# Optimization experiments

Hardware: AMD Instinct MI355X
Metric: run time of the kernel (lower is better)

The kernel has to match this reference:

```python
import jax, jax.numpy as jnp
import numpy as np

N = 50000          # num nodes
E = 1_000_000      # num edges
H = 64             # hidden_dim
IMG, TWT, NUMP, CAT = 512, 768, 16, 8
NCLS, NET = 2, 3   # num_classes, num_edge_types


def setup_inputs() -> dict:
    key = jax.random.key(0)
    ks = jax.random.split(key, 40)
    f32 = jnp.float32
    w = lambda k, s: (jax.random.normal(k, s, f32) * 0.02)
    inp = {
        # forward args
        "image": jax.random.normal(ks[0], (N, IMG), f32),
        "tweets": jax.random.normal(ks[1], (N, TWT), f32),
        "num_prop": jax.random.normal(ks[2], (N, NUMP), f32),
        "category": jax.random.normal(ks[3], (N, CAT), f32),
        "edge_index": jax.random.randint(ks[4], (2, E), 0, N, jnp.int32),
        "edge_type": jax.random.randint(ks[5], (E,), 0, NET, jnp.int32),
        # explicit randomness (replaces randn_like / Bernoulli.sample)
        "eps": jax.random.normal(ks[6], (E, H), f32),
        "u": jax.random.uniform(ks[7], (E,), f32),
        # parameters (stored [in, out]; y = x @ W + b)
        "Wi": w(ks[8], (IMG, H)), "bi": jnp.zeros((H,), f32),
        "Wt": w(ks[9], (TWT, H)), "bt": jnp.zeros((H,), f32),
        "Wn": w(ks[10], (NUMP, H)), "bn": jnp.zeros((H,), f32),
        "Wc": w(ks[11], (CAT, H)), "bc": jnp.zeros((H,), f32),
        "Wf": w(ks[12], (4 * H, H)), "bf": jnp.zeros((H,), f32),
        "Eet": w(ks[13], (NET, 2 * H)),              # edge_type_embed
        "Wmu": w(ks[14], (2 * H, H)), "bmu": jnp.zeros((H,), f32),
        "Wlv": w(ks[15], (2 * H, H)), "blv": jnp.zeros((H,), f32),
        "Wm1": w(ks[16], (2 * H, 64)), "bm1": jnp.zeros((64,), f32),
        "Wm2": w(ks[17], (64, 1)), "bm2": jnp.zeros((1,), f32),
        "Wcls": w(ks[18], (H, NCLS)), "bcls": jnp.zeros((NCLS,), f32),
    }
    return inp


def reference(image, tweets, num_prop, category, edge_index, edge_type, eps, u,
              Wi, bi, Wt, bt, Wn, bn, Wc, bc, Wf, bf, Eet,
              Wmu, bmu, Wlv, blv, Wm1, bm1, Wm2, bm2, Wcls, bcls):
    relu = jax.nn.relu
    # encode_user
    img_f = relu(image @ Wi + bi)
    twt_f = relu(tweets @ Wt + bt)
    num_f = relu(num_prop @ Wn + bn)
    cat_f = relu(category @ Wc + bc)
    node_features = relu(jnp.concatenate([img_f, twt_f, num_f, cat_f], -1) @ Wf + bf)  # [N, H]

    src, dst = edge_index[0], edge_index[1]
    u_i, u_j = node_features[src], node_features[dst]          # [E, H] each
    edge_emb = relu(jnp.concatenate([u_i, u_j], -1) + Eet[edge_type])  # [E, 2H]

    # parameterized_gaussian (z unused downstream, kept for fidelity)
    mu = edge_emb @ Wmu + bmu
    log_var = edge_emb @ Wlv + blv
    z = mu + eps * jnp.exp(0.5 * log_var)

    # edge confidence + Bernoulli sample via inverse-CDF with provided uniforms
    logits_e = (relu(edge_emb @ Wm1 + bm1) @ Wm2 + bm2)[:, 0]  # [E]
    p_ij = jax.nn.sigmoid(logits_e)
    s = (u < p_ij).astype(node_features.dtype)                 # trusted-edge indicator, [E]

    # segment-mean of dst features over trusted edges, grouped by src
    sums = jax.ops.segment_sum(u_j * s[:, None], src, num_segments=N)  # [N, H]
    cnt = jax.ops.segment_sum(s, src, num_segments=N)                  # [N]
    agg = jnp.where(cnt[:, None] > 0, sums / jnp.maximum(cnt, 1.0)[:, None], node_features)

    return agg @ Wcls + bcls  # [N, num_classes]
```

## Files before the change

kernel.cpp:

```cpp
#include <hip/hip_runtime.h>
#include <cstdint>

typedef short short8 __attribute__((ext_vector_type(8)));
typedef float f32x4  __attribute__((ext_vector_type(4)));

__device__ __forceinline__ void split2(float x, short& h, short& l) {
  unsigned u  = __float_as_uint(x);
  unsigned rh = u + 0x7FFFu + ((u >> 16) & 1u);
  h = (short)(rh >> 16);
  float hf = __uint_as_float((rh >> 16) << 16);
  float lf = x - hf;
  unsigned ul = __float_as_uint(lf);
  unsigned rl = ul + 0x7FFFu + ((ul >> 16) & 1u);
  l = (short)(rl >> 16);
}

__device__ __forceinline__ void split4(float4 a, uint2& hp, uint2& lp) {
  unsigned hp0, hp1, lp0, lp1;
  asm("v_cvt_pk_bf16_f32 %0, %1, %2" : "=v"(hp0) : "v"(a.x), "v"(a.y));
  asm("v_cvt_pk_bf16_f32 %0, %1, %2" : "=v"(hp1) : "v"(a.z), "v"(a.w));
  float h0 = __uint_as_float(hp0 << 16);
  float h1 = __uint_as_float(hp0 & 0xFFFF0000u);
  float h2 = __uint_as_float(hp1 << 16);
  float h3 = __uint_as_float(hp1 & 0xFFFF0000u);
  float l0 = a.x - h0, l1 = a.y - h1, l2 = a.z - h2, l3 = a.w - h3;
  asm("v_cvt_pk_bf16_f32 %0, %1, %2" : "=v"(lp0) : "v"(l0), "v"(l1));
  asm("v_cvt_pk_bf16_f32 %0, %1, %2" : "=v"(lp1) : "v"(l2), "v"(l3));
  hp = make_uint2(hp0, hp1);
  lp = make_uint2(lp0, lp1);
}

__global__ __launch_bounds__(256) void init_head(int* __restrict__ head, int N)
{
  const int i = blockIdx.x * 256 + threadIdx.x;
  if (i < N) head[i] = -1;
}

__global__ __launch_bounds__(256) void prep_w(
    const float* __restrict__ Wi, const float* __restrict__ Wt,
    const float* __restrict__ Wn, const float* __restrict__ Wc,
    const float* __restrict__ Wf, const float* __restrict__ Wm1,
    short* __restrict__ hi, short* __restrict__ lo)
{
  int idx = blockIdx.x * 256 + threadIdx.x;
  if (idx >= 1728 * 64) return;
  int kp = idx >> 6, col = idx & 63;
  const float* W; int K, kloc, base;
  if (kp < 512)       { W = Wi;            K = 512; kloc = kp;        base = 0;    }
  else if (kp < 1280) { W = Wt;            K = 768; kloc = kp - 512;  base = 512;  }
  else if (kp < 1312) { W = Wn;            K = 16;  kloc = kp - 1280; base = 1280; }
  else if (kp < 1344) { W = Wc;            K = 8;   kloc = kp - 1312; base = 1312; }
  else if (kp < 1600) { W = Wf;            K = 256; kloc = kp - 1344; base = 1344; }
  else if (kp < 1664) { W = Wm1;           K = 64;  kloc = kp - 1600; base = 1600; }
  else                { W = Wm1 + 64 * 64; K = 64;  kloc = kp - 1664; base = 1664; }
  float x = (kloc < K) ? W[(size_t)kloc * 64 + col] : 0.f;
  short h, l; split2(x, h, l);
  int s = kloc >> 5;
  int addr = ((s * 4 + (col >> 4)) * 64 + ((col & 15) | (((kloc >> 3) & 3) << 4))) * 8 + (kloc & 7);
  size_t o = (size_t)base * 64 + addr;
  hi[o] = h; lo[o] = l;
}

__global__ __launch_bounds__(256) void encoder(
    const float* __restrict__ image, const float* __restrict__ tweets,
    const float* __restrict__ nump, const float* __restrict__ catg,
    const short* __restrict__ Whi, const short* __restrict__ Wlo,
    const float* __restrict__ bi, const float* __restrict__ bt,
    const float* __restrict__ bn, const float* __restrict__ bc,
    const float* __restrict__ bf, float* __restrict__ nf, int M)
{
  __shared__ short Ahi[2][2048];
  __shared__ short Alo[2][2048];
  __shared__ float htile[64 * 68];
  const int tid  = threadIdx.x;
  const int m0   = blockIdx.x * 64;
  const int w    = tid >> 6, l = tid & 63;
  const int srow = tid >> 3;
  const int k0   = (tid & 7) * 4;
  const int i0   = k0 & 7;
  const int kg   = k0 >> 3;

  f32x4 acc2[4];
#pragma unroll
  for (int n = 0; n < 4; n++) acc2[n] = (f32x4){0.f, 0.f, 0.f, 0.f};

  auto stage = [&](const float* A, int lda, int K, int s, int buf) {
#pragma unroll
    for (int r2 = 0; r2 < 2; r2++) {
      const int row  = srow + r2 * 32;
      const int grow = m0 + row;
      const int k    = s * 32 + k0;
      float4 a = make_float4(0.f, 0.f, 0.f, 0.f);
      if (grow < M && k < K) {
        if (k + 3 < K) {
          a = *reinterpret_cast<const float4*>(A + (size_t)grow * lda + k);
        } else {
          a.x = A[(size_t)grow * lda + k];
        }
      }
      uint2 hp, lp; split4(a, hp, lp);
      const int addr = (row >> 4) * 512 + (((row & 15) | (kg << 4)) * 8 + i0);
      *reinterpret_cast<uint2*>(&Ahi[buf][addr]) = hp;
      *reinterpret_cast<uint2*>(&Alo[buf][addr]) = lp;
    }
  };

  auto do_segment = [&](const float* A, int lda, int K, int ksteps,
                        int wstep0, const float* bias, int seg) {
    f32x4 acc[4];
#pragma unroll
    for (int n = 0; n < 4; n++) acc[n] = (f32x4){0.f, 0.f, 0.f, 0.f};

    stage(A, lda, K, 0, 0);
    for (int s = 0; s < ksteps; s++) {
      __syncthreads();
      if (s + 1 < ksteps) stage(A, lda, K, s + 1, (s + 1) & 1);
      const int buf = s & 1;
      short8 ahi = *reinterpret_cast<const short8*>(&Ahi[buf][w * 512 + l * 8]);
      short8 alo = *reinterpret_cast<const short8*>(&Alo[buf][w * 512 + l * 8]);
#pragma unroll
      for (int n = 0; n < 4; n++) {
        short8 whi = *reinterpret_cast<const short8*>(&Whi[((size_t)(wstep0 + s) * 4 + n) * 512 + l * 8]);
        short8 wlo = *reinterpret_cast<const short8*>(&Wlo[((size_t)(wstep0 + s) * 4 + n) * 512 + l * 8]);
        acc[n] = __builtin_amdgcn_mfma_f32_16x16x32_bf16(ahi, whi, acc[n], 0, 0, 0);
        acc[n] = __builtin_amdgcn_mfma_f32_16x16x32_bf16(alo, whi, acc[n], 0, 0, 0);
        acc[n] = __builtin_amdgcn_mfma_f32_16x16x32_bf16(ahi, wlo, acc[n], 0, 0, 0);
      }
    }
    __syncthreads();

#pragma unroll
    for (int n = 0; n < 4; n++) {
      const int c  = n * 16 + (l & 15);
      const float bb = bias[c];
#pragma unroll
      for (int j = 0; j < 4; j++) {
        const int row = w * 16 + (l >> 4) * 4 + j;
        htile[row * 68 + c] = fmaxf(acc[n][j] + bb, 0.f);
      }
    }
    __syncthreads();

#pragma unroll
    for (int ks2 = 0; ks2 < 2; ks2++) {
#pragma unroll
      for (int r2 = 0; r2 < 2; r2++) {
        const int row = srow + r2 * 32;
        float4 a = *reinterpret_cast<const float4*>(&htile[row * 68 + ks2 * 32 + k0]);
        uint2 hp, lp; split4(a, hp, lp);
        const int addr = (row >> 4) * 512 + (((row & 15) | (kg << 4)) * 8 + i0);
        *reinterpret_cast<uint2*>(&Ahi[ks2][addr]) = hp;
        *reinterpret_cast<uint2*>(&Alo[ks2][addr]) = lp;
      }
    }
    __syncthreads();

#pragma unroll
    for (int ks2 = 0; ks2 < 2; ks2++) {
      short8 ahi = *reinterpret_cast<const short8*>(&Ahi[ks2][w * 512 + l * 8]);
      short8 alo = *reinterpret_cast<const short8*>(&Alo[ks2][w * 512 + l * 8]);
      const int st = 42 + seg * 2 + ks2;
#pragma unroll
      for (int n = 0; n < 4; n++) {
        short8 whi = *reinterpret_cast<const short8*>(&Whi[((size_t)st * 4 + n) * 512 + l * 8]);
        short8 wlo = *reinterpret_cast<const short8*>(&Wlo[((size_t)st * 4 + n) * 512 + l * 8]);
        acc2[n] = __builtin_amdgcn_mfma_f32_16x16x32_bf16(ahi, whi, acc2[n], 0, 0, 0);
        acc2[n] = __builtin_amdgcn_mfma_f32_16x16x32_bf16(alo, whi, acc2[n], 0, 0, 0);
        acc2[n] = __builtin_amdgcn_mfma_f32_16x16x32_bf16(ahi, wlo, acc2[n], 0, 0, 0);
      }
    }
    __syncthreads();
  };

  do_segment(image,  512, 512, 16, 0,  bi, 0);
  do_segment(tweets, 768, 768, 24, 16, bt, 1);
  do_segment(nump,   16,  16,  1,  40, bn, 2);
  do_segment(catg,   8,   8,   1,  41, bc, 3);

  const int rb  = m0 + w * 16 + (l >> 4) * 4;
  const int c15 = l & 15;
#pragma unroll
  for (int n = 0; n < 4; n++) {
    const int c = n * 16 + c15;
    const float bb = bf[c];
#pragma unroll
    for (int j = 0; j < 4; j++) {
      const int r = rb + j;
      if (r < M) nf[(size_t)r * 64 + c] = fmaxf(acc2[n][j] + bb, 0.f);
    }
  }
}

__global__ __launch_bounds__(256) void table_kernel(
    const float* __restrict__ nf, const float* __restrict__ Eet,
    const short* __restrict__ Whi, const short* __restrict__ Wlo,
    const float* __restrict__ bm1,
    float* __restrict__ Atab, float* __restrict__ Btab, int N3, int gT)
{
  const bool isB    = (int)blockIdx.x >= gT;
  const int  m0     = (isB ? (int)blockIdx.x - gT : (int)blockIdx.x) * 64;
  const int  eoff   = isB ? 64 : 0;
  const int  wstep0 = isB ? 52 : 50;
  float*     Tab    = isB ? Btab : Atab;

  __shared__ short Ahi[2][2048];
  __shared__ short Alo[2][2048];
  const int tid  = threadIdx.x;
  const int w    = tid >> 6, l = tid & 63;
  const int srow = tid >> 3;
  const int k0   = (tid & 7) * 4;
  const int i0   = k0 & 7;
  const int kg   = k0 >> 3;

#pragma unroll
  for (int ks2 = 0; ks2 < 2; ks2++) {
#pragma unroll
    for (int r2 = 0; r2 < 2; r2++) {
      const int row = srow + r2 * 32;
      const int rg  = m0 + row;
      float4 v = make_float4(0.f, 0.f, 0.f, 0.f);
      if (rg < N3) {
        const int n = rg / 3;
        const int t = rg - n * 3;
        const int k = ks2 * 32 + k0;
        float4 x = *reinterpret_cast<const float4*>(&nf[(size_t)n * 64 + k]);
        float4 e = *reinterpret_cast<const float4*>(&Eet[(size_t)t * 128 + eoff + k]);
        v.x = fmaxf(x.x + e.x, 0.f); v.y = fmaxf(x.y + e.y, 0.f);
        v.z = fmaxf(x.z + e.z, 0.f); v.w = fmaxf(x.w + e.w, 0.f);
      }
      uint2 hp, lp; split4(v, hp, lp);
      const int addr = (row >> 4) * 512 + (((row & 15) | (kg << 4)) * 8 + i0);
      *reinterpret_cast<uint2*>(&Ahi[ks2][addr]) = hp;
      *reinterpret_cast<uint2*>(&Alo[ks2][addr]) = lp;
    }
  }
  __syncthreads();

  f32x4 acc[4];
#pragma unroll
  for (int n = 0; n < 4; n++) acc[n] = (f32x4){0.f, 0.f, 0.f, 0.f};

#pragma unroll
  for (int ks2 = 0; ks2 < 2; ks2++) {
    short8 ahi = *reinterpret_cast<const short8*>(&Ahi[ks2][w * 512 + l * 8]);
    short8 alo = *reinterpret_cast<const short8*>(&Alo[ks2][w * 512 + l * 8]);
#pragma unroll
    for (int n = 0; n < 4; n++) {
      short8 whi = *reinterpret_cast<const short8*>(&Whi[((size_t)(wstep0 + ks2) * 4 + n) * 512 + l * 8]);
      short8 wlo = *reinterpret_cast<const short8*>(&Wlo[((size_t)(wstep0 + ks2) * 4 + n) * 512 + l * 8]);
      acc[n] = __builtin_amdgcn_mfma_f32_16x16x32_bf16(ahi, whi, acc[n], 0, 0, 0);
      acc[n] = __builtin_amdgcn_mfma_f32_16x16x32_bf16(alo, whi, acc[n], 0, 0, 0);
      acc[n] = __builtin_amdgcn_mfma_f32_16x16x32_bf16(ahi, wlo, acc[n], 0, 0, 0);
    }
  }

  const int rb  = m0 + w * 16 + (l >> 4) * 4;
  const int c15 = l & 15;
#pragma unroll
  for (int n = 0; n < 4; n++) {
    const int c = n * 16 + c15;
    const float bb = isB ? 0.f : bm1[c];
#pragma unroll
    for (int j = 0; j < 4; j++) {
      const int r = rb + j;
      if (r < N3) Tab[(size_t)r * 64 + c] = acc[n][j] + bb;
    }
  }
}

__global__ __launch_bounds__(256) void edge_kernel(
    const int* __restrict__ ei, const int* __restrict__ et,
    const float* __restrict__ u,
    const float* __restrict__ Atab, const float* __restrict__ Btab,
    const float* __restrict__ Wm2, const float* __restrict__ bm2,
    int* __restrict__ head, int* __restrict__ nxt, int E)
{
  const int tid = threadIdx.x;
  const int e   = blockIdx.x * 16 + (tid >> 4);
  const int sub = tid & 15;
  if (e >= E) return;

  const int sn = ei[e];
  const int dn = ei[E + e];
  const int t  = et[e];

  float4 a  = *reinterpret_cast<const float4*>(Atab + ((size_t)sn * 3 + t) * 64 + sub * 4);
  float4 b  = *reinterpret_cast<const float4*>(Btab + ((size_t)dn * 3 + t) * 64 + sub * 4);
  float4 wv = *reinterpret_cast<const float4*>(Wm2 + sub * 4);

  float v = fmaxf(a.x + b.x, 0.f) * wv.x;
  v = fmaf(fmaxf(a.y + b.y, 0.f), wv.y, v);
  v = fmaf(fmaxf(a.z + b.z, 0.f), wv.z, v);
  v = fmaf(fmaxf(a.w + b.w, 0.f), wv.w, v);
  v += __shfl_xor(v, 1);
  v += __shfl_xor(v, 2);
  v += __shfl_xor(v, 4);
  v += __shfl_xor(v, 8);

  if (sub == 0) {
    const float p = 1.f / (1.f + expf(-(v + bm2[0])));
    if (u[e] < p) {
      nxt[e] = atomicExch(&head[sn], e);
    }
  }
}

__global__ __launch_bounds__(256) void node_kernel(
    const int* __restrict__ head, const int* __restrict__ nxt,
    const int* __restrict__ ei,
    const float* __restrict__ nf,
    const float* __restrict__ Wcls, const float* __restrict__ bcls,
    float* __restrict__ out, int N, int E)
{
  const int n    = (int)((blockIdx.x * (unsigned)blockDim.x + threadIdx.x) >> 6);
  const int lane = threadIdx.x & 63;
  if (n >= N) return;

  double acc = 0.0;
  int    c   = 0;
  int    e   = head[n];
  while (e >= 0) {
    const int dn = ei[E + e];
    acc += (double)nf[(size_t)dn * 64 + lane];
    c++;
    e = nxt[e];
  }

  const float agg = (c > 0) ? (float)(acc / (double)c) : nf[(size_t)n * 64 + lane];
  float r0 = agg * Wcls[lane * 2 + 0];
  float r1 = agg * Wcls[lane * 2 + 1];
#pragma unroll
  for (int off = 32; off; off >>= 1) {
    r0 += __shfl_xor(r0, off, 64);
    r1 += __shfl_xor(r1, off, 64);
  }
  if (lane == 0) {
    out[(size_t)n * 2 + 0] = r0 + bcls[0];
    out[(size_t)n * 2 + 1] = r1 + bcls[1];
  }
}

extern "C" void kernel_launch(void* const* d_in, const int* in_sizes, int n_in,
                              void* d_out, int out_size, void* d_ws, size_t ws_size,
                              hipStream_t stream)
{
  const float* image    = (const float*)d_in[0];
  const float* tweets   = (const float*)d_in[1];
  const float* num_prop = (const float*)d_in[2];
  const float* category = (const float*)d_in[3];
  const int*   ei       = (const int*)  d_in[4];
  const int*   et       = (const int*)  d_in[5];
  const float* u        = (const float*)d_in[7];
  const float* Wi  = (const float*)d_in[8],  *bi  = (const float*)d_in[9];
  const float* Wt  = (const float*)d_in[10], *bt  = (const float*)d_in[11];
  const float* Wn  = (const float*)d_in[12], *bn  = (const float*)d_in[13];
  const float* Wc  = (const float*)d_in[14], *bc  = (const float*)d_in[15];
  const float* Wf  = (const float*)d_in[16], *bf  = (const float*)d_in[17];
  const float* Eet = (const float*)d_in[18];
  const float* Wm1 = (const float*)d_in[23], *bm1 = (const float*)d_in[24];
  const float* Wm2 = (const float*)d_in[25], *bm2 = (const float*)d_in[26];
  const float* Wcls= (const float*)d_in[27], *bcls= (const float*)d_in[28];
  float* out = (float*)d_out;

  const int N = in_sizes[0] / 512;
  const int E = in_sizes[5];

  float* ws = (float*)d_ws;
  size_t off = 0;
  float* nf     = ws + off;  off += (size_t)N * 64;
  float* Atab   = ws + off;  off += (size_t)N * 3 * 64;
  float* Btab   = ws + off;  off += (size_t)N * 3 * 64;
  int*   head   = (int*)(ws + off);  off += (size_t)N;
  int*   nxt    = (int*)(ws + off);  off += (size_t)E;
  short* Wfhi   = (short*)(ws + off);  off += (1728 * 64) / 2;
  short* Wflo   = (short*)(ws + off);  off += (1728 * 64) / 2;

  init_head<<<(N + 255) / 256, 256, 0, stream>>>(head, N);

  prep_w<<<(1728 * 64 + 255) / 256, 256, 0, stream>>>(Wi, Wt, Wn, Wc, Wf, Wm1,
                                                      Wfhi, Wflo);

  const int gN = (N + 63) / 64;
  encoder<<<gN, 256, 0, stream>>>(image, tweets, num_prop, category,
                                  Wfhi, Wflo, bi, bt, bn, bc, bf, nf, N);

  const int N3 = N * 3;
  const int gT = (N3 + 63) / 64;
  table_kernel<<<2 * gT, 256, 0, stream>>>(nf, Eet, Wfhi, Wflo, bm1,
                                           Atab, Btab, N3, gT);

  edge_kernel<<<(E + 15) / 16, 256, 0, stream>>>(ei, et, u, Atab, Btab,
                                                 Wm2, bm2, head, nxt, E);

  node_kernel<<<(N + 3) / 4, 256, 0, stream>>>(head, nxt, ei, nf, Wcls, bcls,
                                               out, N, E);
}
```

Measured before the change: 328.8 us.

## Pipeline encoder loads via async global-to-LDS copies with four-stage ring buffer

Restructures the encoder GEMM so the raw fp32 input tiles and the pre-split bf16 weight tiles are copied straight into LDS with global_load_lds, using a four-slot ring buffer kept two steps ahead and explicit vmcnt waits. The four input segments are merged into a single 42-step loop. The fp32-to-bf16 hi/lo split now happens after the LDS read instead of before the LDS write, and the rows are XOR-swizzled to avoid bank conflicts. The aim is to hide global memory latency and remove register staging and extra barriers. In exchange it uses 80KB of LDS, which limits occupancy, and it relies on hand-tuned waitcnt counts.

```diff
diff --git a/kernel.cpp b/kernel.cpp
--- a/kernel.cpp
+++ b/kernel.cpp
@@ -28,6 +28,12 @@
   asm("v_cvt_pk_bf16_f32 %0, %1, %2" : "=v"(lp1) : "v"(l2), "v"(l3));
   hp = make_uint2(hp0, hp1);
   lp = make_uint2(lp0, lp1);
+}
+
+__device__ __forceinline__ void gl_lds16(const void* g, void* l) {
+  __builtin_amdgcn_global_load_lds(
+      (const __attribute__((address_space(1))) unsigned int*)g,
+      (__attribute__((address_space(3))) unsigned int*)l, 16, 0, 0);
 }
 
 __global__ __launch_bounds__(256) void init_head(int* __restrict__ head, int N)
@@ -61,6 +67,12 @@
   hi[o] = h; lo[o] = l;
 }
 
+#define ENC_STEPS 42
+#define A_OFF   0
+#define W_OFF   32768
+#define HHI_OFF 65536
+#define HLO_OFF 73728
+
 __global__ __launch_bounds__(256) void encoder(
     const float* __restrict__ image, const float* __restrict__ tweets,
     const float* __restrict__ nump, const float* __restrict__ catg,
@@ -69,96 +81,66 @@
     const float* __restrict__ bn, const float* __restrict__ bc,
     const float* __restrict__ bf, float* __restrict__ nf, int M)
 {
-  __shared__ short Ahi[2][2048];
-  __shared__ short Alo[2][2048];
-  __shared__ float htile[64 * 68];
+  __shared__ uint4 smem4[81920 / 16];
+  char* lds = (char*)smem4;
+
   const int tid  = threadIdx.x;
   const int m0   = blockIdx.x * 64;
   const int w    = tid >> 6, l = tid & 63;
-  const int srow = tid >> 3;
-  const int k0   = (tid & 7) * 4;
-  const int i0   = k0 & 7;
-  const int kg   = k0 >> 3;
-
-  f32x4 acc2[4];
-#pragma unroll
-  for (int n = 0; n < 4; n++) acc2[n] = (f32x4){0.f, 0.f, 0.f, 0.f};
-
-  auto stage = [&](const float* A, int lda, int K, int s, int buf) {
-#pragma unroll
-    for (int r2 = 0; r2 < 2; r2++) {
-      const int row  = srow + r2 * 32;
-      const int grow = m0 + row;
-      const int k    = s * 32 + k0;
-      float4 a = make_float4(0.f, 0.f, 0.f, 0.f);
-      if (grow < M && k < K) {
-        if (k + 3 < K) {
-          a = *reinterpret_cast<const float4*>(A + (size_t)grow * lda + k);
-        } else {
-          a.x = A[(size_t)grow * lda + k];
-        }
+
+  f32x4 acc[4], acc2[4];
+#pragma unroll
+  for (int n = 0; n < 4; n++) {
+    acc[n]  = (f32x4){0.f, 0.f, 0.f, 0.f};
+    acc2[n] = (f32x4){0.f, 0.f, 0.f, 0.f};
+  }
+
+  auto stage = [&](int tt, int b) {
+    const float* As; int lda, kbase, kmax;
+    if (tt < 16)      { As = image;  lda = 512; kbase = tt * 32;        kmax = 7; }
+    else if (tt < 40) { As = tweets; lda = 768; kbase = (tt - 16) * 32; kmax = 7; }
+    else if (tt == 40){ As = nump;   lda = 16;  kbase = 0;              kmax = 3; }
+    else              { As = catg;   lda = 8;   kbase = 0;              kmax = 1; }
+#pragma unroll
+    for (int jj = 0; jj < 2; jj++) {
+      const int j = w * 2 + jj;
+      {
+        int row  = j * 8 + (l >> 3);
+        int grow = m0 + row; if (grow >= M) grow = 0;
+        int cc   = (l & 7) ^ (l >> 3);
+        int k    = (cc <= kmax) ? (kbase + cc * 4) : kbase;
+        gl_lds16(As + (size_t)grow * lda + k, lds + A_OFF + b * 8192 + j * 1024);
       }
-      uint2 hp, lp; split4(a, hp, lp);
-      const int addr = (row >> 4) * 512 + (((row & 15) | (kg << 4)) * 8 + i0);
-      *reinterpret_cast<uint2*>(&Ahi[buf][addr]) = hp;
-      *reinterpret_cast<uint2*>(&Alo[buf][addr]) = lp;
+      {
+        const short* gW = (j < 4) ? (Whi + (size_t)tt * 2048 + j * 512)
+                                  : (Wlo + (size_t)tt * 2048 + (j - 4) * 512);
+        gl_lds16(gW + l * 8, lds + W_OFF + b * 8192 + j * 1024);
+      }
     }
   };
 
-  auto do_segment = [&](const float* A, int lda, int K, int ksteps,
-                        int wstep0, const float* bias, int seg) {
-    f32x4 acc[4];
-#pragma unroll
-    for (int n = 0; n < 4; n++) acc[n] = (f32x4){0.f, 0.f, 0.f, 0.f};
-
-    stage(A, lda, K, 0, 0);
-    for (int s = 0; s < ksteps; s++) {
-      __syncthreads();
-      if (s + 1 < ksteps) stage(A, lda, K, s + 1, (s + 1) & 1);
-      const int buf = s & 1;
-      short8 ahi = *reinterpret_cast<const short8*>(&Ahi[buf][w * 512 + l * 8]);
-      short8 alo = *reinterpret_cast<const short8*>(&Alo[buf][w * 512 + l * 8]);
-#pragma unroll
-      for (int n = 0; n < 4; n++) {
-        short8 whi = *reinterpret_cast<const short8*>(&Whi[((size_t)(wstep0 + s) * 4 + n) * 512 + l * 8]);
-        short8 wlo = *reinterpret_cast<const short8*>(&Wlo[((size_t)(wstep0 + s) * 4 + n) * 512 + l * 8]);
-        acc[n] = __builtin_amdgcn_mfma_f32_16x16x32_bf16(ahi, whi, acc[n], 0, 0, 0);
-        acc[n] = __builtin_amdgcn_mfma_f32_16x16x32_bf16(alo, whi, acc[n], 0, 0, 0);
-        acc[n] = __builtin_amdgcn_mfma_f32_16x16x32_bf16(ahi, wlo, acc[n], 0, 0, 0);
-      }
-    }
-    __syncthreads();
-
+  auto seg2_phase = [&](int seg, const float* bias) {
+    short* hh = (short*)(lds + HHI_OFF);
+    short* hl = (short*)(lds + HLO_OFF);
 #pragma unroll
     for (int n = 0; n < 4; n++) {
-      const int c  = n * 16 + (l & 15);
-      const float bb = bias[c];
+      const int k = n * 16 + (l & 15);
 #pragma unroll
       for (int j = 0; j < 4; j++) {
         const int row = w * 16 + (l >> 4) * 4 + j;
-        htile[row * 68 + c] = fmaxf(acc[n][j] + bb, 0.f);
+        float h = fmaxf(acc[n][j] + bias[k], 0.f);
+        short vh, vl; split2(h, vh, vl);
+        const int addr = (k >> 5) * 2048 + (row >> 4) * 512 +
+                         ((row & 15) | (((k >> 3) & 3) << 4)) * 8 + (k & 7);
+        hh[addr] = vh; hl[addr] = vl;
       }
+      acc[n] = (f32x4){0.f, 0.f, 0.f, 0.f};
     }
     __syncthreads();
-
 #pragma unroll
     for (int ks2 = 0; ks2 < 2; ks2++) {
-#pragma unroll
-      for (int r2 = 0; r2 < 2; r2++) {
-        const int row = srow + r2 * 32;
-        float4 a = *reinterpret_cast<const float4*>(&htile[row * 68 + ks2 * 32 + k0]);
-        uint2 hp, lp; split4(a, hp, lp);
-        const int addr = (row >> 4) * 512 + (((row & 15) | (kg << 4)) * 8 + i0);
-        *reinterpret_cast<uint2*>(&Ahi[ks2][addr]) = hp;
-        *reinterpret_cast<uint2*>(&Alo[ks2][addr]) = lp;
-      }
-    }
-    __syncthreads();
-
-#pragma unroll
-    for (int ks2 = 0; ks2 < 2; ks2++) {
-      short8 ahi = *reinterpret_cast<const short8*>(&Ahi[ks2][w * 512 + l * 8]);
-      short8 alo = *reinterpret_cast<const short8*>(&Alo[ks2][w * 512 + l * 8]);
+      short8 ahi = *reinterpret_cast<const short8*>(&hh[ks2 * 2048 + w * 512 + l * 8]);
+      short8 alo = *reinterpret_cast<const short8*>(&hl[ks2 * 2048 + w * 512 + l * 8]);
       const int st = 42 + seg * 2 + ks2;
 #pragma unroll
       for (int n = 0; n < 4; n++) {
@@ -172,10 +154,47 @@
     __syncthreads();
   };
 
-  do_segment(image,  512, 512, 16, 0,  bi, 0);
-  do_segment(tweets, 768, 768, 24, 16, bt, 1);
-  do_segment(nump,   16,  16,  1,  40, bn, 2);
-  do_segment(catg,   8,   8,   1,  41, bc, 3);
+  stage(0, 0);
+  stage(1, 1);
+
+  for (int t = 0; t < ENC_STEPS; t++) {
+    if (t + 2 < ENC_STEPS) stage(t + 2, (t + 2) & 3);
+    if (t <= ENC_STEPS - 3)      asm volatile("s_waitcnt vmcnt(8)" ::: "memory");
+    else if (t == ENC_STEPS - 2) asm volatile("s_waitcnt vmcnt(4)" ::: "memory");
+    else                         asm volatile("s_waitcnt vmcnt(0)" ::: "memory");
+    __builtin_amdgcn_sched_barrier(0);
+    __builtin_amdgcn_s_barrier();
+    __builtin_amdgcn_sched_barrier(0);
+
+    const int b = t & 3;
+    const char* Ab = lds + A_OFF + b * 8192;
+    const char* Wb = lds + W_OFF + b * 8192;
+    const int row = w * 16 + (l & 15);
+    float4 a0 = *reinterpret_cast<const float4*>(
+        Ab + row * 128 + ((((l >> 4) * 2 + 0) ^ (l & 7)) * 16));
+    float4 a1 = *reinterpret_cast<const float4*>(
+        Ab + row * 128 + ((((l >> 4) * 2 + 1) ^ (l & 7)) * 16));
+    uint2 h01, l01, h23, l23;
+    split4(a0, h01, l01);
+    split4(a1, h23, l23);
+    uint4 ahi_u = make_uint4(h01.x, h01.y, h23.x, h23.y);
+    uint4 alo_u = make_uint4(l01.x, l01.y, l23.x, l23.y);
+    short8 ahi = *reinterpret_cast<short8*>(&ahi_u);
+    short8 alo = *reinterpret_cast<short8*>(&alo_u);
+#pragma unroll
+    for (int n = 0; n < 4; n++) {
+      short8 whi = *reinterpret_cast<const short8*>(Wb + n * 1024 + l * 16);
+      short8 wlo = *reinterpret_cast<const short8*>(Wb + 4096 + n * 1024 + l * 16);
+      acc[n] = __builtin_amdgcn_mfma_f32_16x16x32_bf16(ahi, whi, acc[n], 0, 0, 0);
+      acc[n] = __builtin_amdgcn_mfma_f32_16x16x32_bf16(alo, whi, acc[n], 0, 0, 0);
+      acc[n] = __builtin_amdgcn_mfma_f32_16x16x32_bf16(ahi, wlo, acc[n], 0, 0, 0);
+    }
+
+    if (t == 15)      seg2_phase(0, bi);
+    else if (t == 39) seg2_phase(1, bt);
+    else if (t == 40) seg2_phase(2, bn);
+    else if (t == 41) seg2_phase(3, bc);
+  }
 
   const int rb  = m0 + w * 16 + (l >> 4) * 4;
   const int c15 = l & 15;
```

Result: slower. 443.0 us (+34.7%).
